# Optimization experiments

Hardware: AMD Instinct MI355X
Metric: run time of the kernel (lower is better)

The kernel has to match this reference:

```python
import jax, jax.numpy as jnp
import numpy as np

HEAD_SIZE = 64


def setup_inputs() -> dict:
    key = jax.random.key(0)
    kq, kk, kv, kl = jax.random.split(key, 4)
    B, H, S, D = 2, 12, 512, HEAD_SIZE
    Q = jax.random.normal(kq, (B, H, S, D), dtype=jnp.float32)
    K = jax.random.normal(kk, (B, H, S, D), dtype=jnp.float32)
    V = jax.random.normal(kv, (B, H, S, D), dtype=jnp.float32)
    valid_lens = jax.random.randint(kl, (B, S), 0, S).astype(jnp.int64)
    return {"Q": Q, "K": K, "V": V, "valid_lens": valid_lens}


def reference(Q, K, V, valid_lens):
    # Original torch code repeats K/V across heads so K5[b,i,j] = K[b,j]
    # (and likewise V5), yielding a full heads x heads cross-attention.
    # valid_lens is accepted by the original forward but never used.
    B, H, S, D = Q.shape
    scale = jnp.sqrt(jnp.asarray(D, dtype=Q.dtype))
    # score: [B, H_q, H_kv, S, S]
    score = jnp.einsum('bisd,bjtd->bijst', Q, K) / scale
    attention_weights = jax.nn.softmax(score, axis=-1)
    # per (query-head i, kv-head j) context, then sum over kv heads j
    ctx = jnp.einsum('bijst,bjtd->bisd', attention_weights, V)  # [B,H,S,D]
    context = jnp.transpose(ctx, (0, 2, 1, 3)).reshape(B, S, H * D)
    return context, attention_weights
```

## Files before the change

kernel.cpp:

```cpp
#include <hip/hip_runtime.h>


typedef float    f32x4 __attribute__((ext_vector_type(4)));
typedef float    f32x2 __attribute__((ext_vector_type(2)));
typedef _Float16 f16x8 __attribute__((ext_vector_type(8)));
typedef _Float16 f16x4 __attribute__((ext_vector_type(4)));
typedef _Float16 f16x2 __attribute__((ext_vector_type(2)));

#define MFMA(a, b, c) __builtin_amdgcn_mfma_f32_16x16x32_f16((a), (b), (c), 0, 0, 0)

static __device__ __forceinline__ f16x8 cvt8(f32x4 a, f32x4 b, float sc) {
  f16x8 r;
#pragma unroll
  for (int e = 0; e < 4; ++e) {
    r[e]     = (_Float16)(a[e] * sc);
    r[4 + e] = (_Float16)(b[e] * sc);
  }
  return r;
}

__global__ __launch_bounds__(256) void prep_kernel(
    const float* __restrict__ K, const float* __restrict__ V,
    _Float16* __restrict__ Kh, _Float16* __restrict__ VT)
{
  __shared__ _Float16 tile[64][66];
  const int bid = blockIdx.x, tid = threadIdx.x;
  if (bid < 192) {
    const int bj = bid >> 3, t0 = (bid & 7) << 6;
    const float* vsrc = V + (size_t)(bj * 512 + t0) * 64;
#pragma unroll
    for (int it = 0; it < 16; ++it) {
      int lin = it * 256 + tid;
      int tr = lin >> 6, d = lin & 63;
      tile[tr][d] = (_Float16)vsrc[tr * 64 + d];
    }
    __syncthreads();
#pragma unroll
    for (int it = 0; it < 8; ++it) {
      int lin = it * 512 + tid * 2;
      int d = lin >> 6, tc = lin & 63;
      f16x2 pk = { tile[tc][d], tile[tc + 1][d] };
      *(f16x2*)(VT + ((size_t)(bj * 64 + d) * 512 + t0 + tc)) = pk;
    }
  } else {
    const int base = (bid - 192) * 4096;
#pragma unroll
    for (int it = 0; it < 4; ++it) {
      int idx = base + it * 1024 + tid * 4;
      f32x4 v = *(const f32x4*)(K + idx);
      f16x4 o = { (_Float16)v[0], (_Float16)v[1], (_Float16)v[2], (_Float16)v[3] };
      *(f16x4*)(Kh + idx) = o;
    }
  }
}

__global__ __launch_bounds__(512) void attn_kernel(
    const float* __restrict__ Q, const _Float16* __restrict__ Kh,
    const _Float16* __restrict__ VT, float* __restrict__ ctxo,
    float* __restrict__ wts)
{
  extern __shared__ char smem[];
  __shared__ __attribute__((aligned(16))) float red[2][16][8];

  const int tid = threadIdx.x;
  const int w   = tid >> 6;
  const int l   = tid & 63;
  const int g   = l >> 4;
  const int c16 = l & 15;

  int bb = blockIdx.x;
  const int st = bb & 31; bb >>= 5;
  const int i  = bb % 12;
  const int b  = bb / 12;
  const int s0 = st << 4;

  char* const SB = smem + w * 4096;

  f16x8 aq[2];
  {
    const float* qb = Q + ((size_t)((b * 12 + i) * 512 + s0 + c16)) * 64 + g * 8;
#pragma unroll
    for (int ks = 0; ks < 2; ++ks) {
      const float* p = qb + ks * 32;
      aq[ks] = cvt8(*(const f32x4*)p, *(const f32x4*)(p + 4), 0.125f);
    }
  }

  f32x4 ctx[4] = {};
  const size_t bi12 = (size_t)(b * 12 + i) * 12;

  for (int j = 0; j < 12; ++j) {
    f32x4 acc[4] = {};
    {
      const _Float16* kb = Kh + ((size_t)((b * 12 + j) * 512 + w * 64 + c16)) * 64 + g * 8;
#pragma unroll
      for (int c = 0; c < 4; ++c) {
        f16x8 bk0 = *(const f16x8*)(kb + c * 1024);
        f16x8 bk1 = *(const f16x8*)(kb + c * 1024 + 32);
        acc[c] = MFMA(aq[0], bk0, acc[c]);
        acc[c] = MFMA(aq[1], bk1, acc[c]);
      }
    }

    float inv[4];
#pragma unroll
    for (int c = 0; c < 4; ++c)
#pragma unroll
      for (int r = 0; r < 4; ++r) acc[c][r] = __expf(acc[c][r]);
#pragma unroll
    for (int r = 0; r < 4; ++r) {
      float v = acc[0][r] + acc[1][r] + acc[2][r] + acc[3][r];
      v += __shfl_xor(v, 1);
      v += __shfl_xor(v, 2);
      v += __shfl_xor(v, 4);
      v += __shfl_xor(v, 8);
      inv[r] = v;
    }
    const int jp = j & 1;
    if (c16 == 0) {
#pragma unroll
      for (int r = 0; r < 4; ++r) red[jp][g * 4 + r][w] = inv[r];
    }
    __syncthreads();
#pragma unroll
    for (int r = 0; r < 4; ++r) {
      f32x4 q0 = *(const f32x4*)&red[jp][g * 4 + r][0];
      f32x4 q1 = *(const f32x4*)&red[jp][g * 4 + r][4];
      inv[r] = 1.0f / (q0[0] + q0[1] + q0[2] + q0[3] + q1[0] + q1[1] + q1[2] + q1[3]);
    }

#pragma unroll
    for (int c = 0; c < 4; ++c)
#pragma unroll
      for (int r = 0; r < 4; ++r) {
        float wv = acc[c][r] * inv[r];
        int s = g * 4 + r, t = c * 16 + c16;
        *(_Float16*)(SB + ((s * 128 + t * 2) ^ ((s & 7) << 4))) = (_Float16)wv;
      }

    {
      float* wb = wts + ((bi12 + j) << 18) + (size_t)s0 * 512 + w * 64;
#pragma unroll
      for (int it = 0; it < 2; ++it) {
        int lin = it * 64 + l;
        int row = lin >> 3, o8 = lin & 7;
        int swz = (row & 7) << 4;
        f16x4 h0 = *(const f16x4*)(SB + ((row * 128 + o8 * 8) ^ swz));
        f16x4 h1 = *(const f16x4*)(SB + ((row * 128 + o8 * 8 + 64) ^ swz));
        f32x4 o0 = { (float)h0[0], (float)h0[1], (float)h0[2], (float)h0[3] };
        f32x4 o1 = { (float)h1[0], (float)h1[1], (float)h1[2], (float)h1[3] };
        __builtin_nontemporal_store(o0, (f32x4*)(wb + row * 512 + o8 * 4));
        __builtin_nontemporal_store(o1, (f32x4*)(wb + row * 512 + o8 * 4 + 32));
      }
    }

    {
      const _Float16* vtb = VT + (size_t)((b * 12 + j) * 64) * 512 + w * 64;
#pragma unroll
      for (int kk = 0; kk < 2; ++kk) {
        f16x8 am = *(const f16x8*)(SB + ((c16 * 128 + kk * 64 + g * 16) ^ ((c16 & 7) << 4)));
#pragma unroll
        for (int n = 0; n < 4; ++n) {
          f16x8 bv = *(const f16x8*)(vtb + (size_t)(n * 16 + c16) * 512 + kk * 32 + g * 8);
          ctx[n] = MFMA(am, bv, ctx[n]);
        }
      }
    }
  }

#pragma unroll
  for (int n = 0; n < 4; ++n)
#pragma unroll
    for (int r = 0; r < 4; ++r)
      *(float*)(SB + (g * 4 + r) * 256 + (n * 16 + c16) * 4) = ctx[n][r];
  __syncthreads();
  {
    int s = tid >> 5, d2 = (tid & 31) * 2;
    f32x2 a2 = { 0.f, 0.f };
#pragma unroll
    for (int w8 = 0; w8 < 8; ++w8)
      a2 += *(const f32x2*)(smem + w8 * 4096 + s * 256 + d2 * 4);
    float* ob = ctxo + ((size_t)b * 512 + s0 + s) * 768 + i * 64 + d2;
    __builtin_nontemporal_store(a2, (f32x2*)ob);
  }
}

extern "C" void kernel_launch(void* const* d_in, const int* in_sizes, int n_in,
                              void* d_out, int out_size, void* d_ws, size_t ws_size,
                              hipStream_t stream) {
  const float* Q = (const float*)d_in[0];
  const float* K = (const float*)d_in[1];
  const float* V = (const float*)d_in[2];
  float* out = (float*)d_out;
  float* ctx = out;
  float* wts = out + 786432;

  _Float16* Kh = (_Float16*)d_ws;
  _Float16* VT = Kh + 2 * 12 * 512 * 64;

  prep_kernel<<<dim3(384), dim3(256), 0, stream>>>(K, V, Kh, VT);
  attn_kernel<<<dim3(768), dim3(512), 32768, stream>>>(Q, Kh, VT, ctx, wts);
}
```

Baseline: 410.0 us.

## Halve waves per block, defer softmax normalization past PV MFMA, stage V through LDS

The attention kernel now runs 4 waves per block, each handling 128 keys instead of 64. The P·V product uses unnormalized exponentials, so the MFMA work no longer waits on the cross-wave row-sum barrier; normalization is applied afterwards to the per-head context and to the stored weights. V tiles are copied into swizzled LDS before the MFMA, and the 1/sqrt(d) scale moves into the K fp16 conversion in the prep kernel. The trade-offs are more LDS per block (48KB), more registers per wave, and an extra per-head fp32 accumulator.

```diff
diff --git a/kernel.cpp b/kernel.cpp
--- a/kernel.cpp
+++ b/kernel.cpp
@@ -2,19 +2,18 @@
 
 
 typedef float    f32x4 __attribute__((ext_vector_type(4)));
-typedef float    f32x2 __attribute__((ext_vector_type(2)));
 typedef _Float16 f16x8 __attribute__((ext_vector_type(8)));
 typedef _Float16 f16x4 __attribute__((ext_vector_type(4)));
 typedef _Float16 f16x2 __attribute__((ext_vector_type(2)));
 
 #define MFMA(a, b, c) __builtin_amdgcn_mfma_f32_16x16x32_f16((a), (b), (c), 0, 0, 0)
 
-static __device__ __forceinline__ f16x8 cvt8(f32x4 a, f32x4 b, float sc) {
+static __device__ __forceinline__ f16x8 cvt8(f32x4 a, f32x4 b) {
   f16x8 r;
 #pragma unroll
   for (int e = 0; e < 4; ++e) {
-    r[e]     = (_Float16)(a[e] * sc);
-    r[4 + e] = (_Float16)(b[e] * sc);
+    r[e]     = (_Float16)a[e];
+    r[4 + e] = (_Float16)b[e];
   }
   return r;
 }
@@ -48,19 +47,20 @@
     for (int it = 0; it < 4; ++it) {
       int idx = base + it * 1024 + tid * 4;
       f32x4 v = *(const f32x4*)(K + idx);
-      f16x4 o = { (_Float16)v[0], (_Float16)v[1], (_Float16)v[2], (_Float16)v[3] };
+      f16x4 o = { (_Float16)(v[0] * 0.125f), (_Float16)(v[1] * 0.125f),
+                  (_Float16)(v[2] * 0.125f), (_Float16)(v[3] * 0.125f) };
       *(f16x4*)(Kh + idx) = o;
     }
   }
 }
 
-__global__ __launch_bounds__(512) void attn_kernel(
+__global__ __launch_bounds__(256, 3) void attn_kernel(
     const float* __restrict__ Q, const _Float16* __restrict__ Kh,
     const _Float16* __restrict__ VT, float* __restrict__ ctxo,
     float* __restrict__ wts)
 {
   extern __shared__ char smem[];
-  __shared__ __attribute__((aligned(16))) float red[2][16][8];
+  __shared__ __attribute__((aligned(16))) float red[2][16][4];
 
   const int tid = threadIdx.x;
   const int w   = tid >> 6;
@@ -74,7 +74,8 @@
   const int b  = bb / 12;
   const int s0 = st << 4;
 
-  char* const SB = smem + w * 4096;
+  char* const VB = smem + w * 12288;
+  char* const SB = VB + 8192;
 
   f16x8 aq[2];
   {
@@ -82,7 +83,7 @@
 #pragma unroll
     for (int ks = 0; ks < 2; ++ks) {
       const float* p = qb + ks * 32;
-      aq[ks] = cvt8(*(const f32x4*)p, *(const f32x4*)(p + 4), 0.125f);
+      aq[ks] = cvt8(*(const f32x4*)p, *(const f32x4*)(p + 4));
     }
   }
 
@@ -90,11 +91,12 @@
   const size_t bi12 = (size_t)(b * 12 + i) * 12;
 
   for (int j = 0; j < 12; ++j) {
-    f32x4 acc[4] = {};
-    {
-      const _Float16* kb = Kh + ((size_t)((b * 12 + j) * 512 + w * 64 + c16)) * 64 + g * 8;
-#pragma unroll
-      for (int c = 0; c < 4; ++c) {
+    const int jp = j & 1;
+    f32x4 acc[8] = {};
+    {
+      const _Float16* kb = Kh + ((size_t)((b * 12 + j) * 512 + w * 128 + c16)) * 64 + g * 8;
+#pragma unroll
+      for (int c = 0; c < 8; ++c) {
         f16x8 bk0 = *(const f16x8*)(kb + c * 1024);
         f16x8 bk1 = *(const f16x8*)(kb + c * 1024 + 32);
         acc[c] = MFMA(aq[0], bk0, acc[c]);
@@ -102,86 +104,104 @@
       }
     }
 
-    float inv[4];
-#pragma unroll
-    for (int c = 0; c < 4; ++c)
+#pragma unroll
+    for (int c = 0; c < 8; ++c)
 #pragma unroll
       for (int r = 0; r < 4; ++r) acc[c][r] = __expf(acc[c][r]);
+
 #pragma unroll
     for (int r = 0; r < 4; ++r) {
-      float v = acc[0][r] + acc[1][r] + acc[2][r] + acc[3][r];
+      float v = acc[0][r];
+#pragma unroll
+      for (int c = 1; c < 8; ++c) v += acc[c][r];
       v += __shfl_xor(v, 1);
       v += __shfl_xor(v, 2);
       v += __shfl_xor(v, 4);
       v += __shfl_xor(v, 8);
-      inv[r] = v;
-    }
-    const int jp = j & 1;
-    if (c16 == 0) {
-#pragma unroll
-      for (int r = 0; r < 4; ++r) red[jp][g * 4 + r][w] = inv[r];
-    }
+      if (c16 == 0) red[jp][g * 4 + r][w] = v;
+    }
+
+#pragma unroll
+    for (int c = 0; c < 8; ++c)
+#pragma unroll
+      for (int r = 0; r < 4; ++r) {
+        int s = g * 4 + r, t = c * 16 + c16;
+        *(_Float16*)(SB + ((s * 256 + t * 2) ^ ((s & 7) << 4))) = (_Float16)acc[c][r];
+      }
+
+    f32x4 ctxj[4] = {};
+    {
+      const _Float16* vtb = VT + (size_t)((b * 12 + j) * 64) * 512 + w * 128;
+#pragma unroll
+      for (int h = 0; h < 2; ++h) {
+#pragma unroll
+        for (int it = 0; it < 8; ++it) {
+          int blk = it * 64 + l;
+          int d = blk >> 3, tc = (blk & 7) * 8;
+          f16x8 v = *(const f16x8*)(vtb + (size_t)d * 512 + h * 64 + tc);
+          *(f16x8*)(VB + ((d * 128 + tc * 2) ^ ((d & 7) << 4))) = v;
+        }
+#pragma unroll
+        for (int ksl = 0; ksl < 2; ++ksl) {
+          const int ltoff = (ksl * 32 + g * 8) * 2;
+          f16x8 am = *(const f16x8*)(SB + ((c16 * 256 + h * 128 + ltoff) ^ ((c16 & 7) << 4)));
+#pragma unroll
+          for (int n = 0; n < 4; ++n) {
+            int d = n * 16 + c16;
+            f16x8 bv = *(const f16x8*)(VB + ((d * 128 + ltoff) ^ ((d & 7) << 4)));
+            ctxj[n] = MFMA(am, bv, ctxj[n]);
+          }
+        }
+      }
+    }
+
     __syncthreads();
+
+    {
+      float inv[4];
+#pragma unroll
+      for (int r = 0; r < 4; ++r) {
+        f32x4 q4 = *(const f32x4*)(&red[jp][g * 4 + r][0]);
+        inv[r] = __builtin_amdgcn_rcpf(q4[0] + q4[1] + q4[2] + q4[3]);
+      }
+#pragma unroll
+      for (int n = 0; n < 4; ++n)
+#pragma unroll
+        for (int r = 0; r < 4; ++r) ctx[n][r] += inv[r] * ctxj[n][r];
+    }
+
+    {
+      float* wbase = wts + ((bi12 + j) << 18) + (size_t)s0 * 512 + w * 128;
+#pragma unroll
+      for (int it = 0; it < 8; ++it) {
+        int row = it * 2 + (l >> 5);
+        int t0  = (l & 31) * 4;
+        f16x4 h4 = *(const f16x4*)(SB + ((row * 256 + t0 * 2) ^ ((row & 7) << 4)));
+        f32x4 q4 = *(const f32x4*)(&red[jp][row][0]);
+        float iv = __builtin_amdgcn_rcpf(q4[0] + q4[1] + q4[2] + q4[3]);
+        f32x4 o4 = { (float)h4[0] * iv, (float)h4[1] * iv,
+                     (float)h4[2] * iv, (float)h4[3] * iv };
+        __builtin_nontemporal_store(o4, (f32x4*)(wbase + (size_t)row * 512 + t0));
+      }
+    }
+  }
+
+#pragma unroll
+  for (int n = 0; n < 4; ++n)
 #pragma unroll
     for (int r = 0; r < 4; ++r) {
-      f32x4 q0 = *(const f32x4*)&red[jp][g * 4 + r][0];
-      f32x4 q1 = *(const f32x4*)&red[jp][g * 4 + r][4];
-      inv[r] = 1.0f / (q0[0] + q0[1] + q0[2] + q0[3] + q1[0] + q1[1] + q1[2] + q1[3]);
-    }
-
-#pragma unroll
-    for (int c = 0; c < 4; ++c)
-#pragma unroll
-      for (int r = 0; r < 4; ++r) {
-        float wv = acc[c][r] * inv[r];
-        int s = g * 4 + r, t = c * 16 + c16;
-        *(_Float16*)(SB + ((s * 128 + t * 2) ^ ((s & 7) << 4))) = (_Float16)wv;
-      }
-
-    {
-      float* wb = wts + ((bi12 + j) << 18) + (size_t)s0 * 512 + w * 64;
-#pragma unroll
-      for (int it = 0; it < 2; ++it) {
-        int lin = it * 64 + l;
-        int row = lin >> 3, o8 = lin & 7;
-        int swz = (row & 7) << 4;
-        f16x4 h0 = *(const f16x4*)(SB + ((row * 128 + o8 * 8) ^ swz));
-        f16x4 h1 = *(const f16x4*)(SB + ((row * 128 + o8 * 8 + 64) ^ swz));
-        f32x4 o0 = { (float)h0[0], (float)h0[1], (float)h0[2], (float)h0[3] };
-        f32x4 o1 = { (float)h1[0], (float)h1[1], (float)h1[2], (float)h1[3] };
-        __builtin_nontemporal_store(o0, (f32x4*)(wb + row * 512 + o8 * 4));
-        __builtin_nontemporal_store(o1, (f32x4*)(wb + row * 512 + o8 * 4 + 32));
-      }
-    }
-
-    {
-      const _Float16* vtb = VT + (size_t)((b * 12 + j) * 64) * 512 + w * 64;
-#pragma unroll
-      for (int kk = 0; kk < 2; ++kk) {
-        f16x8 am = *(const f16x8*)(SB + ((c16 * 128 + kk * 64 + g * 16) ^ ((c16 & 7) << 4)));
-#pragma unroll
-        for (int n = 0; n < 4; ++n) {
-          f16x8 bv = *(const f16x8*)(vtb + (size_t)(n * 16 + c16) * 512 + kk * 32 + g * 8);
-          ctx[n] = MFMA(am, bv, ctx[n]);
-        }
-      }
-    }
-  }
-
-#pragma unroll
-  for (int n = 0; n < 4; ++n)
-#pragma unroll
-    for (int r = 0; r < 4; ++r)
-      *(float*)(SB + (g * 4 + r) * 256 + (n * 16 + c16) * 4) = ctx[n][r];
+      int s = g * 4 + r, d = n * 16 + c16;
+      *(float*)(VB + (s * 256 + d * 4)) = ctx[n][r];
+    }
   __syncthreads();
   {
-    int s = tid >> 5, d2 = (tid & 31) * 2;
-    f32x2 a2 = { 0.f, 0.f };
-#pragma unroll
-    for (int w8 = 0; w8 < 8; ++w8)
-      a2 += *(const f32x2*)(smem + w8 * 4096 + s * 256 + d2 * 4);
-    float* ob = ctxo + ((size_t)b * 512 + s0 + s) * 768 + i * 64 + d2;
-    __builtin_nontemporal_store(a2, (f32x2*)ob);
+    int s = tid >> 4, d4 = (tid & 15) * 4;
+    f32x4 A = {0.f, 0.f, 0.f, 0.f};
+#pragma unroll
+    for (int w4 = 0; w4 < 4; ++w4)
+      A += *(const f32x4*)(smem + w4 * 12288 + s * 256 + d4 * 4);
+    float* ob = ctxo + ((size_t)b * 512 + s0 + s) * 768 + i * 64 + d4;
+    __builtin_nontemporal_store(A, (f32x4*)ob);
   }
 }
 
@@ -199,5 +219,5 @@
   _Float16* VT = Kh + 2 * 12 * 512 * 64;
 
   prep_kernel<<<dim3(384), dim3(256), 0, stream>>>(K, V, Kh, VT);
-  attn_kernel<<<dim3(768), dim3(512), 32768, stream>>>(Q, Kh, VT, ctx, wts);
-}
+  attn_kernel<<<dim3(768), dim3(256), 49152, stream>>>(Q, Kh, VT, ctx, wts);
+}
```

Result: faster. 378.9 us (-7.6%).
